# Kernel tuning notes

Hardware: AMD Instinct MI355X
Metric: run time of the kernel (lower is better)

Reference implementation:

```python
import jax, jax.numpy as jnp
import numpy as np
import math

B, S, D_MODEL, H = 2, 2048, 1024, 16
HD = D_MODEL // H  # head_dim = 64


def _rope(x, seq_len):
    # x: [B, S, H, HD]; standard rotate-half RoPE with base 10000
    d = x.shape[-1]
    inv_freq = 1.0 / (10000.0 ** (jnp.arange(0, d, 2, dtype=jnp.float32) / d))
    t = jnp.arange(seq_len, dtype=jnp.float32)
    freqs = t[:, None] * inv_freq[None, :]              # [S, HD/2]
    emb = jnp.concatenate([freqs, freqs], axis=-1)      # [S, HD]
    cos = jnp.cos(emb)[None, :, None, :]
    sin = jnp.sin(emb)[None, :, None, :]
    x1, x2 = jnp.split(x, 2, axis=-1)
    rot = jnp.concatenate([-x2, x1], axis=-1)
    return x * cos + rot * sin


def setup_inputs() -> dict:
    key = jax.random.key(0)
    ks = jax.random.split(key, 11)
    s = 1.0 / math.sqrt(D_MODEL)
    return {
        "query": jax.random.normal(ks[0], (B, S, D_MODEL), jnp.float32),
        "keys": jax.random.normal(ks[1], (B, S, D_MODEL), jnp.float32),
        "values": jax.random.normal(ks[2], (B, S, D_MODEL), jnp.float32),
        "Wq": jax.random.normal(ks[3], (D_MODEL, D_MODEL), jnp.float32) * s,
        "bq": jnp.zeros((D_MODEL,), jnp.float32),
        "Wk": jax.random.normal(ks[4], (D_MODEL, D_MODEL), jnp.float32) * s,
        "bk": jnp.zeros((D_MODEL,), jnp.float32),
        "Wv": jax.random.normal(ks[5], (D_MODEL, D_MODEL), jnp.float32) * s,
        "bv": jnp.zeros((D_MODEL,), jnp.float32),
        "Wo": jax.random.normal(ks[6], (D_MODEL, D_MODEL), jnp.float32) * s,
        "bo": jnp.zeros((D_MODEL,), jnp.float32),
    }


def reference(query, keys, values, Wq, bq, Wk, bk, Wv, bv, Wo, bo):
    b, s, _ = query.shape
    scale = math.sqrt(HD)
    q = (query @ Wq.T + bq).reshape(b, s, H, HD)   # [B,S,H,HD]
    k = (keys @ Wk.T + bk).reshape(b, s, H, HD)
    v = (values @ Wv.T + bv).reshape(b, s, H, HD)
    q = _rope(q, s)
    k = _rope(k, s)
    # scores: [B,H,Sq,Sk]
    scores = jnp.einsum('bqhd,bkhd->bhqk', q, k)
    causal = jnp.tril(jnp.ones((s, s), dtype=bool))[None, None]
    scores = jnp.where(causal, scores, -jnp.inf) / scale
    attn = jax.nn.softmax(scores, axis=-1)
    ctx = jnp.einsum('bhqk,bkhd->bqhd', attn, v).reshape(b, s, H * HD)
    out = ctx @ Wo.T + bo
    return out, attn
```

## Files before the change

kernel.cpp:

```cpp
#include <hip/hip_runtime.h>
#include <hip/hip_bf16.h>
#include <stdint.h>
#include <math.h>


typedef __attribute__((ext_vector_type(8))) __bf16 bf16x8;
typedef __attribute__((ext_vector_type(4))) float f32x4;

__device__ __forceinline__ unsigned short f2bf(float f) {
  unsigned int u = __float_as_uint(f);
  u += 0x7fffu + ((u >> 16) & 1u);
  return (unsigned short)(u >> 16);
}

typedef const __attribute__((address_space(1))) unsigned int* gas_ptr;
typedef __attribute__((address_space(3))) unsigned int* las_ptr;
__device__ __forceinline__ void glds16(const void* g, void* l) {
  __builtin_amdgcn_global_load_lds((gas_ptr)g, (las_ptr)l, 16, 0, 0);
}

__global__ __launch_bounds__(256) void rope_table(float2* __restrict__ tab) {
  const int i = blockIdx.x * 256 + threadIdx.x;
  const int spos = i >> 5, d = i & 31;
  const double invf = pow(10000.0, -(double)d / 32.0);
  const double ang = (double)spos * invf;
  double sn, cs;
  sincos(ang, &sn, &cs);
  tab[i] = make_float2((float)cs, (float)sn);
}

__global__ __launch_bounds__(256) void cvt_all(
    const float* __restrict__ a0, const float* __restrict__ a1,
    const float* __restrict__ a2, const float* __restrict__ w0,
    const float* __restrict__ w1, const float* __restrict__ w2,
    const float* __restrict__ w3, unsigned short* __restrict__ ws) {
  const int z = blockIdx.z;
  const float* src;
  unsigned short* dst;
  int n;
  if (z == 0)      { src = a0; dst = ws;             n = 4194304; }
  else if (z == 1) { src = a1; dst = ws + 4194304;   n = 4194304; }
  else if (z == 2) { src = a2; dst = ws + 8388608;   n = 4194304; }
  else if (z == 3) { src = w0; dst = ws + 12582912;  n = 1048576; }
  else if (z == 4) { src = w1; dst = ws + 13631488;  n = 1048576; }
  else if (z == 5) { src = w2; dst = ws + 14680064;  n = 1048576; }
  else             { src = w3; dst = ws + 15728640;  n = 1048576; }
  const int n4 = n >> 2;
  for (int i = blockIdx.x * 256 + threadIdx.x; i < n4; i += gridDim.x * 256) {
    float4 f = ((const float4*)src)[i];
    ushort4 u;
    u.x = f2bf(f.x); u.y = f2bf(f.y); u.z = f2bf(f.z); u.w = f2bf(f.w);
    ((ushort4*)dst)[i] = u;
  }
}

__global__ __launch_bounds__(256) void gemm_qkv(
    const unsigned short* __restrict__ xq, const unsigned short* __restrict__ xk,
    const unsigned short* __restrict__ xv, const unsigned short* __restrict__ wq,
    const unsigned short* __restrict__ wk, const unsigned short* __restrict__ wv,
    const float* __restrict__ bq, const float* __restrict__ bk,
    const float* __restrict__ bv, const float2* __restrict__ rtab,
    unsigned short* __restrict__ qo, unsigned short* __restrict__ ko,
    unsigned short* __restrict__ vo) {
  const int z = blockIdx.z;
  const unsigned short* A = (z == 0) ? xq : (z == 1) ? xk : xv;
  const unsigned short* W = (z == 0) ? wq : (z == 1) ? wk : wv;
  const float* bias = (z == 0) ? bq : (z == 1) ? bk : bv;
  unsigned short* out = (z == 0) ? qo : (z == 1) ? ko : vo;

  const int t = threadIdx.x;
  const int lane = t & 63, wave = t >> 6;
  const int wr = wave >> 1, wc = wave & 1;
  const int lrow = lane & 15, lkb = lane >> 4;
  const int m0 = blockIdx.y * 128, n0 = blockIdx.x * 128;

  __shared__ __align__(16) unsigned short abuf[4096];
  __shared__ __align__(16) unsigned short bbuf[4096];

  f32x4 acc[4][4] = {};

  for (int k0 = 0; k0 < 1024; k0 += 32) {
    __syncthreads();
#pragma unroll
    for (int i = 0; i < 2; ++i) {
      int slot = i * 256 + t;
      int kb = slot >> 7, row = slot & 127;
      glds16(A + (size_t)(m0 + row) * 1024 + k0 + kb * 8, &abuf[slot * 8]);
      glds16(W + (size_t)(n0 + row) * 1024 + k0 + kb * 8, &bbuf[slot * 8]);
    }
    __syncthreads();
    bf16x8 af[4], bfr[4];
#pragma unroll
    for (int mi = 0; mi < 4; ++mi)
      af[mi] = *(const bf16x8*)&abuf[(lkb * 128 + wr * 64 + mi * 16 + lrow) * 8];
#pragma unroll
    for (int ni = 0; ni < 4; ++ni)
      bfr[ni] = *(const bf16x8*)&bbuf[(lkb * 128 + wc * 64 + ni * 16 + lrow) * 8];
#pragma unroll
    for (int mi = 0; mi < 4; ++mi)
#pragma unroll
      for (int ni = 0; ni < 4; ++ni)
        acc[mi][ni] = __builtin_amdgcn_mfma_f32_16x16x32_bf16(af[mi], bfr[ni],
                                                              acc[mi][ni], 0, 0, 0);
  }

  const int nbase = n0 + wc * 64;
  float bias_v[4];
#pragma unroll
  for (int ni = 0; ni < 4; ++ni) bias_v[ni] = bias[nbase + ni * 16 + lrow];

  const int mbase = m0 + wr * 64 + 4 * lkb;
  const bool rope = (z < 2);
  const float qsc = (z == 0) ? 0.125f : 1.0f;

#pragma unroll
  for (int mi = 0; mi < 4; ++mi) {
#pragma unroll
    for (int r = 0; r < 4; ++r) {
      const int m = mbase + mi * 16 + r;
      const int bidx = m >> 11, spos = m & 2047;
      float vals[4];
#pragma unroll
      for (int ni = 0; ni < 4; ++ni) vals[ni] = acc[mi][ni][r] + bias_v[ni];
      if (rope) {
#pragma unroll
        for (int ni = 0; ni < 2; ++ni) {
          const int d = ni * 16 + lrow;
          const float2 cs2 = rtab[spos * 32 + d];
          float x1 = vals[ni], x2 = vals[ni + 2];
          vals[ni] = (x1 * cs2.x - x2 * cs2.y) * qsc;
          vals[ni + 2] = (x2 * cs2.x + x1 * cs2.y) * qsc;
        }
      }
#pragma unroll
      for (int ni = 0; ni < 4; ++ni) {
        const int n = nbase + ni * 16 + lrow;
        const int h = n >> 6, d = n & 63;
        out[(size_t)((bidx * 16 + h) * 2048 + spos) * 64 + d] = f2bf(vals[ni]);
      }
    }
  }
}

__global__ __launch_bounds__(256) void gemm_out(
    const unsigned short* __restrict__ A, const unsigned short* __restrict__ W,
    const float* __restrict__ bias, float* __restrict__ out) {
  const int t = threadIdx.x;
  const int lane = t & 63, wave = t >> 6;
  const int wr = wave >> 1, wc = wave & 1;
  const int lrow = lane & 15, lkb = lane >> 4;
  const int m0 = blockIdx.y * 128, n0 = blockIdx.x * 128;

  __shared__ __align__(16) unsigned short abuf[4096];
  __shared__ __align__(16) unsigned short bbuf[4096];

  f32x4 acc[4][4] = {};

  for (int k0 = 0; k0 < 1024; k0 += 32) {
    __syncthreads();
#pragma unroll
    for (int i = 0; i < 2; ++i) {
      int slot = i * 256 + t;
      int kb = slot >> 7, row = slot & 127;
      glds16(A + (size_t)(m0 + row) * 1024 + k0 + kb * 8, &abuf[slot * 8]);
      glds16(W + (size_t)(n0 + row) * 1024 + k0 + kb * 8, &bbuf[slot * 8]);
    }
    __syncthreads();
    bf16x8 af[4], bfr[4];
#pragma unroll
    for (int mi = 0; mi < 4; ++mi)
      af[mi] = *(const bf16x8*)&abuf[(lkb * 128 + wr * 64 + mi * 16 + lrow) * 8];
#pragma unroll
    for (int ni = 0; ni < 4; ++ni)
      bfr[ni] = *(const bf16x8*)&bbuf[(lkb * 128 + wc * 64 + ni * 16 + lrow) * 8];
#pragma unroll
    for (int mi = 0; mi < 4; ++mi)
#pragma unroll
      for (int ni = 0; ni < 4; ++ni)
        acc[mi][ni] = __builtin_amdgcn_mfma_f32_16x16x32_bf16(af[mi], bfr[ni],
                                                              acc[mi][ni], 0, 0, 0);
  }

  const int nbase = n0 + wc * 64;
  float bias_v[4];
#pragma unroll
  for (int ni = 0; ni < 4; ++ni) bias_v[ni] = bias[nbase + ni * 16 + lrow];
  const int mbase = m0 + wr * 64 + 4 * lkb;
#pragma unroll
  for (int mi = 0; mi < 4; ++mi)
#pragma unroll
    for (int r = 0; r < 4; ++r) {
      const int m = mbase + mi * 16 + r;
      float* orow = out + (size_t)m * 1024 + nbase;
#pragma unroll
      for (int ni = 0; ni < 4; ++ni)
        orow[ni * 16 + lrow] = acc[mi][ni][r] + bias_v[ni];
    }
}

__global__ __launch_bounds__(256) void transpose_v(
    const unsigned short* __restrict__ v, unsigned short* __restrict__ vt) {
  const int s0 = blockIdx.x * 64;
  const int bh = blockIdx.y;
  __shared__ __align__(16) unsigned short tile[64][80];
  const int t = threadIdx.x;
  {
    const int row = t >> 2, cb = t & 3;
    const unsigned short* src = v + (size_t)(bh * 2048 + s0 + row) * 64 + cb * 16;
    *(uint4*)&tile[row][cb * 16] = *(const uint4*)src;
    *(uint4*)&tile[row][cb * 16 + 8] = *(const uint4*)(src + 8);
  }
  __syncthreads();
  {
    const int d = t >> 2, sc = t & 3;
    __align__(16) unsigned short tmp[16];
#pragma unroll
    for (int u = 0; u < 16; ++u) tmp[u] = tile[sc * 16 + u][d];
    unsigned short* dst = vt + (size_t)(bh * 64 + d) * 2048 + s0 + sc * 16;
    *(uint4*)dst = *(const uint4*)&tmp[0];
    *(uint4*)(dst + 8) = *(const uint4*)&tmp[8];
  }
}

__global__ __launch_bounds__(256) void attn_kernel(
    const unsigned short* __restrict__ Q, const unsigned short* __restrict__ Km,
    const unsigned short* __restrict__ Vt, float* __restrict__ attn,
    unsigned short* __restrict__ ctx) {
  const int qt = blockIdx.x;
  const int bh = blockIdx.y;
  const int t = threadIdx.x;
  const int lane = t & 63, wave = t >> 6;
  const int lrow = lane & 15, lg = lane >> 4;
  const int q0 = qt * 64;
  const int wq0 = q0 + wave * 16;

  const unsigned short* Qb = Q + (size_t)bh * 2048 * 64;
  const unsigned short* Kb = Km + (size_t)bh * 2048 * 64;
  const unsigned short* Vb = Vt + (size_t)bh * 64 * 2048;
  float* attn_b = attn + (size_t)bh * 2048 * 2048;

  __shared__ __align__(16) unsigned short kbuf[4096];
  __shared__ __align__(16) unsigned short vbuf[4096];
  __shared__ __align__(16) unsigned short pbuf[4][1024];

  bf16x8 qf[2];
#pragma unroll
  for (int dk = 0; dk < 2; ++dk)
    qf[dk] = *(const bf16x8*)(Qb + (size_t)(wq0 + lrow) * 64 + dk * 32 + lg * 8);

  const int nkt = qt + 1;
  float l_loc[4] = {0.f, 0.f, 0.f, 0.f};

  auto lupdate = [&](const unsigned short* buf, int kbase) {
    f32x4 s[4] = {};
#pragma unroll
    for (int fc = 0; fc < 4; ++fc)
#pragma unroll
      for (int dk = 0; dk < 2; ++dk) {
        bf16x8 kf = *(const bf16x8*)&buf[((dk * 4 + lg) * 64 + fc * 16 + lrow) * 8];
        s[fc] = __builtin_amdgcn_mfma_f32_16x16x32_bf16(qf[dk], kf, s[fc], 0, 0, 0);
      }
#pragma unroll
    for (int r = 0; r < 4; ++r) {
      const int qg = wq0 + 4 * lg + r;
      float sum = 0.f;
#pragma unroll
      for (int fc = 0; fc < 4; ++fc) {
        const int kg = kbase + fc * 16 + lrow;
        sum += __expf((kg <= qg) ? s[fc][r] : -1e30f);
      }
      l_loc[r] += sum;
    }
  };

  for (int kt = 0; kt < nkt; kt += 2) {
    const int k0 = kt * 64;
    const bool two = (kt + 1) < nkt;
    __syncthreads();
#pragma unroll
    for (int i = 0; i < 2; ++i) {
      int slot = i * 256 + t;
      int cb = slot >> 6, row = slot & 63;
      glds16(Kb + (size_t)(k0 + row) * 64 + cb * 8, &kbuf[slot * 8]);
      if (two)
        glds16(Kb + (size_t)(k0 + 64 + row) * 64 + cb * 8, &vbuf[slot * 8]);
    }
    __syncthreads();
    lupdate(kbuf, k0);
    if (two) lupdate(vbuf, k0 + 64);
  }

  float loglinv[4];
#pragma unroll
  for (int r = 0; r < 4; ++r) {
    float l = l_loc[r];
#pragma unroll
    for (int off = 1; off < 16; off <<= 1) l += __shfl_xor(l, off);
    loglinv[r] = -__logf(l);
  }

  f32x4 oa[4] = {};
  for (int kt = 0; kt < nkt; ++kt) {
    const int k0 = kt * 64;
    __syncthreads();
#pragma unroll
    for (int i = 0; i < 2; ++i) {
      int slot = i * 256 + t;
      int kb = slot >> 6, row = slot & 63;
      glds16(Kb + (size_t)(k0 + row) * 64 + kb * 8, &kbuf[slot * 8]);
      glds16(Vb + (size_t)row * 2048 + k0 + kb * 8, &vbuf[slot * 8]);
    }
    __syncthreads();
    f32x4 s[4] = {};
#pragma unroll
    for (int fc = 0; fc < 4; ++fc)
#pragma unroll
      for (int dk = 0; dk < 2; ++dk) {
        bf16x8 kf = *(const bf16x8*)&kbuf[((dk * 4 + lg) * 64 + fc * 16 + lrow) * 8];
        s[fc] = __builtin_amdgcn_mfma_f32_16x16x32_bf16(qf[dk], kf, s[fc], 0, 0, 0);
      }
#pragma unroll
    for (int r = 0; r < 4; ++r) {
      const int qg = wq0 + 4 * lg + r;
      const int q_ = 4 * lg + r;
      float* arow = attn_b + (size_t)qg * 2048 + k0;
#pragma unroll
      for (int fc = 0; fc < 4; ++fc) {
        const int kg = k0 + fc * 16 + lrow;
        const float p = (kg <= qg) ? __expf(s[fc][r] + loglinv[r]) : 0.f;
        arow[fc * 16 + lrow] = p;
        const int k_ = fc * 16 + lrow;
        const int dl = q_ + 16 * ((k_ >> 3) & 3);
        const int kk = k_ >> 5, j = k_ & 7;
        int byteo = (kk * 64 + dl) * 16 + j * 2;
        byteo ^= ((kk * 8 + (dl >> 3)) & 7) << 4;
        *(unsigned short*)((char*)pbuf[wave] + byteo) = f2bf(p);
      }
    }
#pragma unroll
    for (int kk = 0; kk < 2; ++kk) {
      int rbyte = (kk * 64 + lane) * 16;
      rbyte ^= ((kk * 8 + (lane >> 3)) & 7) << 4;
      bf16x8 pa = *(const bf16x8*)((char*)pbuf[wave] + rbyte);
#pragma unroll
      for (int fd = 0; fd < 4; ++fd) {
        bf16x8 vf = *(const bf16x8*)&vbuf[((kk * 4 + lg) * 64 + fd * 16 + lrow) * 8];
        oa[fd] = __builtin_amdgcn_mfma_f32_16x16x32_bf16(pa, vf, oa[fd], 0, 0, 0);
      }
    }
  }

  const int zc0 = nkt * 16;
  for (int rr = 0; rr < 16; ++rr) {
    const int qg = wq0 + rr;
    float4* arow = (float4*)(attn_b + (size_t)qg * 2048);
    for (int c = zc0 + lane; c < 512; c += 64)
      arow[c] = make_float4(0.f, 0.f, 0.f, 0.f);
  }

  const int bidx = bh >> 4, h = bh & 15;
#pragma unroll
  for (int fd = 0; fd < 4; ++fd)
#pragma unroll
    for (int r = 0; r < 4; ++r) {
      const int qg = wq0 + 4 * lg + r;
      ctx[(size_t)(bidx * 2048 + qg) * 1024 + h * 64 + fd * 16 + lrow] =
          f2bf(oa[fd][r]);
    }
}

extern "C" void kernel_launch(void* const* d_in, const int* in_sizes, int n_in,
                              void* d_out, int out_size, void* d_ws, size_t ws_size,
                              hipStream_t stream) {
  const float* q_in = (const float*)d_in[0];
  const float* k_in = (const float*)d_in[1];
  const float* v_in = (const float*)d_in[2];
  const float* Wq = (const float*)d_in[3];
  const float* bq = (const float*)d_in[4];
  const float* Wk = (const float*)d_in[5];
  const float* bk = (const float*)d_in[6];
  const float* Wv = (const float*)d_in[7];
  const float* bv = (const float*)d_in[8];
  const float* Wo = (const float*)d_in[9];
  const float* bo = (const float*)d_in[10];

  unsigned short* ws = (unsigned short*)d_ws;
  float* outp = (float*)d_out;

  const size_t OXQ = 0, OXK = 4194304, OXV = 8388608;
  const size_t OWQ = 12582912, OWK = 13631488, OWV = 14680064, OWO = 15728640;
  const size_t OQ = 16777216, OK = 20971520, OV = 25165824;
  const size_t OTAB = 29360128;
  const size_t OVT = OXK;
  const size_t OCTX = OXQ;
  float2* rtab = (float2*)(ws + OTAB);

  rope_table<<<dim3(256), 256, 0, stream>>>(rtab);
  cvt_all<<<dim3(512, 1, 7), 256, 0, stream>>>(q_in, k_in, v_in, Wq, Wk, Wv, Wo, ws);
  gemm_qkv<<<dim3(8, 32, 3), 256, 0, stream>>>(ws + OXQ, ws + OXK, ws + OXV,
                                               ws + OWQ, ws + OWK, ws + OWV,
                                               bq, bk, bv, rtab,
                                               ws + OQ, ws + OK, ws + OV);
  transpose_v<<<dim3(32, 32), 256, 0, stream>>>(ws + OV, ws + OVT);
  attn_kernel<<<dim3(32, 32), 256, 0, stream>>>(ws + OQ, ws + OK, ws + OVT,
                                                outp + 4194304, ws + OCTX);
  gemm_out<<<dim3(8, 32), 256, 0, stream>>>(ws + OCTX, ws + OWO, bo, outp);
}
```

Measured before the change: 353.6 us.

## Pair complementary causal query tiles per block to balance work and share K/V loads

Each attention block now handles two query tiles, p and 31-p, so every block does the same number of key tiles under the causal mask. It also loads each K/V tile once and reuses it for both query tiles. The grid is halved to 512 blocks, which lowers parallelism, and doubled register state (two Q fragments and two accumulators) may reduce occupancy.

```diff
diff --git a/kernel.cpp b/kernel.cpp
--- a/kernel.cpp
+++ b/kernel.cpp
@@ -226,13 +226,14 @@
     const unsigned short* __restrict__ Q, const unsigned short* __restrict__ Km,
     const unsigned short* __restrict__ Vt, float* __restrict__ attn,
     unsigned short* __restrict__ ctx) {
-  const int qt = blockIdx.x;
+  const int p = blockIdx.x;
+  const int qta = p, qtb = 31 - p;
   const int bh = blockIdx.y;
   const int t = threadIdx.x;
   const int lane = t & 63, wave = t >> 6;
   const int lrow = lane & 15, lg = lane >> 4;
-  const int q0 = qt * 64;
-  const int wq0 = q0 + wave * 16;
+  const int wq0a = qta * 64 + wave * 16;
+  const int wq0b = qtb * 64 + wave * 16;
 
   const unsigned short* Qb = Q + (size_t)bh * 2048 * 64;
   const unsigned short* Kb = Km + (size_t)bh * 2048 * 64;
@@ -243,15 +244,18 @@
   __shared__ __align__(16) unsigned short vbuf[4096];
   __shared__ __align__(16) unsigned short pbuf[4][1024];
 
-  bf16x8 qf[2];
-#pragma unroll
-  for (int dk = 0; dk < 2; ++dk)
-    qf[dk] = *(const bf16x8*)(Qb + (size_t)(wq0 + lrow) * 64 + dk * 32 + lg * 8);
-
-  const int nkt = qt + 1;
-  float l_loc[4] = {0.f, 0.f, 0.f, 0.f};
-
-  auto lupdate = [&](const unsigned short* buf, int kbase) {
+  bf16x8 qfa[2], qfb[2];
+#pragma unroll
+  for (int dk = 0; dk < 2; ++dk) {
+    qfa[dk] = *(const bf16x8*)(Qb + (size_t)(wq0a + lrow) * 64 + dk * 32 + lg * 8);
+    qfb[dk] = *(const bf16x8*)(Qb + (size_t)(wq0b + lrow) * 64 + dk * 32 + lg * 8);
+  }
+
+  float l_a[4] = {0.f, 0.f, 0.f, 0.f};
+  float l_b[4] = {0.f, 0.f, 0.f, 0.f};
+
+  auto lupdate = [&](const unsigned short* buf, int kbase, int wq0,
+                     const bf16x8* qf, float* l_loc) {
     f32x4 s[4] = {};
 #pragma unroll
     for (int fc = 0; fc < 4; ++fc)
@@ -273,9 +277,9 @@
     }
   };
 
-  for (int kt = 0; kt < nkt; kt += 2) {
+  for (int kt = 0; kt <= qtb; kt += 2) {
     const int k0 = kt * 64;
-    const bool two = (kt + 1) < nkt;
+    const bool two = (kt + 1) <= qtb;
     __syncthreads();
 #pragma unroll
     for (int i = 0; i < 2; ++i) {
@@ -286,31 +290,32 @@
         glds16(Kb + (size_t)(k0 + 64 + row) * 64 + cb * 8, &vbuf[slot * 8]);
     }
     __syncthreads();
-    lupdate(kbuf, k0);
-    if (two) lupdate(vbuf, k0 + 64);
-  }
-
-  float loglinv[4];
+    if (kt <= qta) lupdate(kbuf, k0, wq0a, qfa, l_a);
+    lupdate(kbuf, k0, wq0b, qfb, l_b);
+    if (two) {
+      if (kt + 1 <= qta) lupdate(vbuf, k0 + 64, wq0a, qfa, l_a);
+      lupdate(vbuf, k0 + 64, wq0b, qfb, l_b);
+    }
+  }
+
+  float loglinva[4], loglinvb[4];
 #pragma unroll
   for (int r = 0; r < 4; ++r) {
-    float l = l_loc[r];
-#pragma unroll
-    for (int off = 1; off < 16; off <<= 1) l += __shfl_xor(l, off);
-    loglinv[r] = -__logf(l);
-  }
-
-  f32x4 oa[4] = {};
-  for (int kt = 0; kt < nkt; ++kt) {
-    const int k0 = kt * 64;
-    __syncthreads();
-#pragma unroll
-    for (int i = 0; i < 2; ++i) {
-      int slot = i * 256 + t;
-      int kb = slot >> 6, row = slot & 63;
-      glds16(Kb + (size_t)(k0 + row) * 64 + kb * 8, &kbuf[slot * 8]);
-      glds16(Vb + (size_t)row * 2048 + k0 + kb * 8, &vbuf[slot * 8]);
-    }
-    __syncthreads();
+    float la = l_a[r], lb = l_b[r];
+#pragma unroll
+    for (int off = 1; off < 16; off <<= 1) {
+      la += __shfl_xor(la, off);
+      lb += __shfl_xor(lb, off);
+    }
+    loglinva[r] = -__logf(la);
+    loglinvb[r] = -__logf(lb);
+  }
+
+  f32x4 oaa[4] = {};
+  f32x4 oab[4] = {};
+
+  auto process = [&](int k0, int wq0, const bf16x8* qf, const float* loglinv,
+                     f32x4* oa) {
     f32x4 s[4] = {};
 #pragma unroll
     for (int fc = 0; fc < 4; ++fc)
@@ -327,14 +332,14 @@
 #pragma unroll
       for (int fc = 0; fc < 4; ++fc) {
         const int kg = k0 + fc * 16 + lrow;
-        const float p = (kg <= qg) ? __expf(s[fc][r] + loglinv[r]) : 0.f;
-        arow[fc * 16 + lrow] = p;
+        const float pv = (kg <= qg) ? __expf(s[fc][r] + loglinv[r]) : 0.f;
+        arow[fc * 16 + lrow] = pv;
         const int k_ = fc * 16 + lrow;
         const int dl = q_ + 16 * ((k_ >> 3) & 3);
         const int kk = k_ >> 5, j = k_ & 7;
         int byteo = (kk * 64 + dl) * 16 + j * 2;
         byteo ^= ((kk * 8 + (dl >> 3)) & 7) << 4;
-        *(unsigned short*)((char*)pbuf[wave] + byteo) = f2bf(p);
+        *(unsigned short*)((char*)pbuf[wave] + byteo) = f2bf(pv);
       }
     }
 #pragma unroll
@@ -348,14 +353,36 @@
         oa[fd] = __builtin_amdgcn_mfma_f32_16x16x32_bf16(pa, vf, oa[fd], 0, 0, 0);
       }
     }
-  }
-
-  const int zc0 = nkt * 16;
-  for (int rr = 0; rr < 16; ++rr) {
-    const int qg = wq0 + rr;
-    float4* arow = (float4*)(attn_b + (size_t)qg * 2048);
-    for (int c = zc0 + lane; c < 512; c += 64)
-      arow[c] = make_float4(0.f, 0.f, 0.f, 0.f);
+  };
+
+  for (int kt = 0; kt <= qtb; ++kt) {
+    const int k0 = kt * 64;
+    __syncthreads();
+#pragma unroll
+    for (int i = 0; i < 2; ++i) {
+      int slot = i * 256 + t;
+      int cb = slot >> 6, row = slot & 63;
+      glds16(Kb + (size_t)(k0 + row) * 64 + cb * 8, &kbuf[slot * 8]);
+      glds16(Vb + (size_t)row * 2048 + k0 + cb * 8, &vbuf[slot * 8]);
+    }
+    __syncthreads();
+    if (kt <= qta) process(k0, wq0a, qfa, loglinva, oaa);
+    process(k0, wq0b, qfb, loglinvb, oab);
+  }
+
+  {
+    const int zc0a = (qta + 1) * 16;
+    for (int rr = 0; rr < 16; ++rr) {
+      float4* arow = (float4*)(attn_b + (size_t)(wq0a + rr) * 2048);
+      for (int c = zc0a + lane; c < 512; c += 64)
+        arow[c] = make_float4(0.f, 0.f, 0.f, 0.f);
+    }
+    const int zc0b = (qtb + 1) * 16;
+    for (int rr = 0; rr < 16; ++rr) {
+      float4* arow = (float4*)(attn_b + (size_t)(wq0b + rr) * 2048);
+      for (int c = zc0b + lane; c < 512; c += 64)
+        arow[c] = make_float4(0.f, 0.f, 0.f, 0.f);
+    }
   }
 
   const int bidx = bh >> 4, h = bh & 15;
@@ -363,9 +390,12 @@
   for (int fd = 0; fd < 4; ++fd)
 #pragma unroll
     for (int r = 0; r < 4; ++r) {
-      const int qg = wq0 + 4 * lg + r;
-      ctx[(size_t)(bidx * 2048 + qg) * 1024 + h * 64 + fd * 16 + lrow] =
-          f2bf(oa[fd][r]);
+      const int qga = wq0a + 4 * lg + r;
+      const int qgb = wq0b + 4 * lg + r;
+      ctx[(size_t)(bidx * 2048 + qga) * 1024 + h * 64 + fd * 16 + lrow] =
+          f2bf(oaa[fd][r]);
+      ctx[(size_t)(bidx * 2048 + qgb) * 1024 + h * 64 + fd * 16 + lrow] =
+          f2bf(oab[fd][r]);
     }
 }
 
@@ -402,7 +432,7 @@
                                                bq, bk, bv, rtab,
                                                ws + OQ, ws + OK, ws + OV);
   transpose_v<<<dim3(32, 32), 256, 0, stream>>>(ws + OV, ws + OVT);
-  attn_kernel<<<dim3(32, 32), 256, 0, stream>>>(ws + OQ, ws + OK, ws + OVT,
+  attn_kernel<<<dim3(16, 32), 256, 0, stream>>>(ws + OQ, ws + OK, ws + OVT,
                                                 outp + 4194304, ws + OCTX);
   gemm_out<<<dim3(8, 32), 256, 0, stream>>>(ws + OCTX, ws + OWO, bo, outp);
 }
```

Measured after the change: 318.7 us. -9.9%, faster.
